# Performance work log

Measured on AMD Instinct MI355X. Metric: run time of the kernel, lower is better.

The kernel has to match this reference:

```python
import jax, jax.numpy as jnp
import numpy as np

DIM = 1024
NUM_HEADS = 16
HEAD_DIM = DIM // NUM_HEADS
SCALE = HEAD_DIM ** (-0.5)


def setup_inputs() -> dict:
    key = jax.random.key(0)
    ks = jax.random.split(key, 5)
    b, n = 4, 1370
    x = jax.random.normal(ks[0], (b, n, DIM), dtype=jnp.float32)
    # Dense kernels: Keras Dense stores kernel as [in, out]
    w_qkv = jax.random.normal(ks[1], (DIM, 3 * DIM), dtype=jnp.float32) * (DIM ** -0.5)
    b_qkv = jnp.zeros((3 * DIM,), dtype=jnp.float32)
    w_proj = jax.random.normal(ks[2], (DIM, DIM), dtype=jnp.float32) * (DIM ** -0.5)
    b_proj = jnp.zeros((DIM,), dtype=jnp.float32)
    return {"x": x, "w_qkv": w_qkv, "b_qkv": b_qkv, "w_proj": w_proj, "b_proj": b_proj}


def reference(x, w_qkv, b_qkv, w_proj, b_proj):
    b, n, _ = x.shape
    qkv = x @ w_qkv + b_qkv                       # [b, n, 3*dim]
    qkv = qkv.reshape(b, n, 3, NUM_HEADS, HEAD_DIM)
    qkv = jnp.transpose(qkv, (2, 0, 3, 1, 4))     # [3, b, h, n, d]
    q, k, v = qkv[0], qkv[1], qkv[2]
    q = q * jnp.asarray(SCALE, dtype=q.dtype)
    attn = jnp.einsum("bhqd,bhkd->bhqk", q, k)    # [b, h, n, n]
    attn = jax.nn.softmax(attn, axis=-1)
    out = jnp.einsum("bhqk,bhkd->bhqd", attn, v)  # [b, h, n, d]
    out = jnp.transpose(out, (0, 2, 1, 3)).reshape(b, n, DIM)
    return out @ w_proj + b_proj
```

## Files before the change

kernel.cpp:

```cpp
#include <hip/hip_runtime.h>
#include <stdint.h>
#include <math.h>

typedef __attribute__((ext_vector_type(8))) __bf16 bf16x8;
typedef __attribute__((ext_vector_type(4))) __bf16 bf16x4;
typedef __attribute__((ext_vector_type(4))) float f32x4;
typedef __attribute__((ext_vector_type(8))) short short8;

#define MFMA(a, b, c) __builtin_amdgcn_mfma_f32_16x16x32_bf16((a), (b), (c), 0, 0, 0)

constexpr int DIMC  = 1024;
constexpr int HEADS = 16;
constexpr int HD    = 64;
constexpr int BATCH = 4;
constexpr int SEQ   = 1370;
constexpr int MROWS = BATCH * SEQ;
constexpr int NPAD  = 1408;
constexpr float QK_SCALE = 0.125f * 1.44269504088896341f;

__device__ __forceinline__ unsigned short f2bf(float f) {
    union { float f; unsigned int u; } v; v.f = f;
    unsigned int r = (v.u + 0x7FFFu + ((v.u >> 16) & 1u)) >> 16;
    return (unsigned short)r;
}

__device__ __forceinline__ void gl2lds16(const unsigned short* g, unsigned short* l) {
    __builtin_amdgcn_global_load_lds(
        (const __attribute__((address_space(1))) unsigned int*)g,
        (__attribute__((address_space(3))) unsigned int*)l,
        16, 0, 0);
}

__global__ void cast_x_kernel(const float* __restrict__ x, unsigned short* __restrict__ xb, int nvec) {
    int i = blockIdx.x * blockDim.x + threadIdx.x;
    if (i >= nvec) return;
    f32x4 a = reinterpret_cast<const f32x4*>(x)[2 * i];
    f32x4 b = reinterpret_cast<const f32x4*>(x)[2 * i + 1];
    short8 o;
    o[0] = (short)f2bf(a[0]); o[1] = (short)f2bf(a[1]);
    o[2] = (short)f2bf(a[2]); o[3] = (short)f2bf(a[3]);
    o[4] = (short)f2bf(b[0]); o[5] = (short)f2bf(b[1]);
    o[6] = (short)f2bf(b[2]); o[7] = (short)f2bf(b[3]);
    reinterpret_cast<short8*>(xb)[i] = o;
}

__global__ __launch_bounds__(256) void transpose_cast_kernel(const float* __restrict__ in,
                                                             unsigned short* __restrict__ out,
                                                             int R, int C) {
    __shared__ float tile[32][33];
    int tx = threadIdx.x & 31, ty = threadIdx.x >> 5;
    int cbase = blockIdx.x * 32, rbase = blockIdx.y * 32;
#pragma unroll
    for (int rr = 0; rr < 4; ++rr) {
        int r = ty + rr * 8;
        tile[r][tx] = in[(size_t)(rbase + r) * C + cbase + tx];
    }
    __syncthreads();
#pragma unroll
    for (int rr = 0; rr < 4; ++rr) {
        int cr = ty + rr * 8;
        out[(size_t)(cbase + cr) * R + rbase + tx] = f2bf(tile[tx][cr]);
    }
}

__global__ void zero_vpad_kernel(unsigned short* __restrict__ vTg) {
    int idx = blockIdx.x * blockDim.x + threadIdx.x;
    const int padw = NPAD - SEQ;
    const int total = 64 * 64 * padw;
    if (idx >= total) return;
    int col = SEQ + idx % padw;
    int rowflat = idx / padw;
    vTg[(size_t)rowflat * NPAD + col] = 0;
}

template <int EPI>
__global__ __launch_bounds__(256) void gemm_bt_kernel(const unsigned short* __restrict__ A,
                                                      const unsigned short* __restrict__ Bt,
                                                      int M, int N, int K,
                                                      const float* __restrict__ bias,
                                                      unsigned short* __restrict__ qg,
                                                      unsigned short* __restrict__ kg,
                                                      unsigned short* __restrict__ vTg,
                                                      float* __restrict__ outf) {
    __shared__ unsigned short As[128 * 32];
    __shared__ unsigned short Bs[128 * 32];
    const int tid = threadIdx.x;
    const int l = tid & 63, w = tid >> 6;
    const int wr = w >> 1, wc = w & 1;
    const int lm = l & 15, lk = l >> 4;
    const int brow = blockIdx.y * 128, bcol = blockIdx.x * 128;

    f32x4 acc[4][4];
#pragma unroll
    for (int i = 0; i < 4; ++i)
#pragma unroll
        for (int j = 0; j < 4; ++j) acc[i][j] = f32x4{0.f, 0.f, 0.f, 0.f};

    const int nkt = K >> 5;
    for (int kt = 0; kt < nkt; ++kt) {
#pragma unroll
        for (int rr = 0; rr < 2; ++rr) {
            int flat = rr * 256 + tid;
            int row = flat >> 2;
            int c8 = (flat & 3) << 3;
            int ga = min(brow + row, M - 1);
            gl2lds16(&A[(size_t)ga * K + kt * 32 + c8], &As[flat * 8]);
            int gb = bcol + row;
            gl2lds16(&Bt[(size_t)gb * K + kt * 32 + c8], &Bs[flat * 8]);
        }
        __syncthreads();
        bf16x8 af[4], bfr[4];
#pragma unroll
        for (int i = 0; i < 4; ++i)
            af[i] = *reinterpret_cast<const bf16x8*>(&As[(wr * 64 + i * 16 + lm) * 32 + lk * 8]);
#pragma unroll
        for (int j = 0; j < 4; ++j)
            bfr[j] = *reinterpret_cast<const bf16x8*>(&Bs[(wc * 64 + j * 16 + lm) * 32 + lk * 8]);
#pragma unroll
        for (int i = 0; i < 4; ++i)
#pragma unroll
            for (int j = 0; j < 4; ++j)
                acc[i][j] = MFMA(af[i], bfr[j], acc[i][j]);
        __syncthreads();
    }

#pragma unroll
    for (int i = 0; i < 4; ++i) {
        int mbase = brow + wr * 64 + i * 16 + lk * 4;
#pragma unroll
        for (int j = 0; j < 4; ++j) {
            int col = bcol + wc * 64 + j * 16 + lm;
            float bv = bias[col];
#pragma unroll
            for (int r = 0; r < 4; ++r) {
                int m = mbase + r;
                if (m >= M) continue;
                float val = acc[i][j][r] + bv;
                if constexpr (EPI == 0) {
                    int which = col >> 10;
                    int head = (col >> 6) & 15;
                    int d = col & 63;
                    int b = m / SEQ;
                    int nseq = m - b * SEQ;
                    int bh = b * HEADS + head;
                    if (which == 0) {
                        qg[((size_t)bh * SEQ + nseq) * HD + d] = f2bf(val * QK_SCALE);
                    } else if (which == 1) {
                        kg[((size_t)bh * SEQ + nseq) * HD + d] = f2bf(val);
                    } else {
                        vTg[((size_t)bh * HD + d) * NPAD + nseq] = f2bf(val);
                    }
                } else {
                    outf[(size_t)m * DIMC + col] = val;
                }
            }
        }
    }
}

__global__ __launch_bounds__(256) void attn_kernel(const unsigned short* __restrict__ qg,
                                                   const unsigned short* __restrict__ kg,
                                                   const unsigned short* __restrict__ vTg,
                                                   unsigned short* __restrict__ ao) {
    __shared__ unsigned short Ks[64 * 72];
    __shared__ unsigned short Vs[64 * 72];
    __shared__ unsigned short Pw[4][16 * 72];

    const int tid = threadIdx.x;
    const int l = tid & 63, w = tid >> 6;
    const int lm = l & 15, lk = l >> 4;

    int wg = (blockIdx.x & 7) * 176 + (blockIdx.x >> 3);
    const int bh = wg / 22;
    const int qbase = (wg - bh * 22) * 64;

    int qr = min(qbase + w * 16 + lm, SEQ - 1);
    const unsigned short* qp = &qg[((size_t)bh * SEQ + qr) * HD + lk * 8];
    bf16x8 qf0 = *reinterpret_cast<const bf16x8*>(qp);
    bf16x8 qf1 = *reinterpret_cast<const bf16x8*>(qp + 32);

    f32x4 o[4];
#pragma unroll
    for (int jd = 0; jd < 4; ++jd) o[jd] = f32x4{0.f, 0.f, 0.f, 0.f};
    float mrun = -INFINITY, lrun = 0.f;

    const int r0 = tid >> 3;
    const int c8b = (tid & 7) << 3;
    const unsigned short* kbase = &kg[(size_t)bh * SEQ * HD];
    const unsigned short* vbase = &vTg[(size_t)bh * HD * NPAD];

    auto load_tile = [&](int t, short8* kr, short8* vr) {
#pragma unroll
        for (int rr = 0; rr < 2; ++rr) {
            int row = rr * 32 + r0;
            int kvg = min(t * 64 + row, SEQ - 1);
            kr[rr] = *reinterpret_cast<const short8*>(&kbase[(size_t)kvg * HD + c8b]);
            vr[rr] = *reinterpret_cast<const short8*>(&vbase[(size_t)row * NPAD + t * 64 + c8b]);
        }
    };
    auto write_tile = [&](const short8* kr, const short8* vr) {
#pragma unroll
        for (int rr = 0; rr < 2; ++rr) {
            int row = rr * 32 + r0;
            *reinterpret_cast<short8*>(&Ks[row * 72 + c8b]) = kr[rr];
            *reinterpret_cast<short8*>(&Vs[row * 72 + c8b]) = vr[rr];
        }
    };

    const int NT = (SEQ + 63) >> 6;

    auto compute_tile = [&](int t) {
        f32x4 s[4];
        __builtin_amdgcn_s_setprio(1);
#pragma unroll
        for (int j = 0; j < 4; ++j) {
            f32x4 z = {0.f, 0.f, 0.f, 0.f};
            bf16x8 k0 = *reinterpret_cast<const bf16x8*>(&Ks[(j * 16 + lm) * 72 + lk * 8]);
            bf16x8 k1 = *reinterpret_cast<const bf16x8*>(&Ks[(j * 16 + lm) * 72 + 32 + lk * 8]);
            z = MFMA(k0, qf0, z);
            z = MFMA(k1, qf1, z);
            s[j] = z;
        }
        __builtin_amdgcn_s_setprio(0);

        if (t == NT - 1) {
#pragma unroll
            for (int j = 0; j < 4; ++j)
#pragma unroll
                for (int r = 0; r < 4; ++r) {
                    int kvg = t * 64 + j * 16 + lk * 4 + r;
                    if (kvg >= SEQ) s[j][r] = -INFINITY;
                }
        }

        float tmax = s[0][0];
#pragma unroll
        for (int j = 0; j < 4; ++j)
#pragma unroll
            for (int r = 0; r < 4; ++r) tmax = fmaxf(tmax, s[j][r]);
        tmax = fmaxf(tmax, __shfl_xor(tmax, 16));
        tmax = fmaxf(tmax, __shfl_xor(tmax, 32));

        if (!__all(tmax - mrun <= 8.0f)) {
            float mnew = fmaxf(mrun, tmax);
            float scale = exp2f(mrun - mnew);
            mrun = mnew;
            lrun *= scale;
            float sc[4];
#pragma unroll
            for (int r = 0; r < 4; ++r) sc[r] = __shfl(scale, lk * 4 + r);
#pragma unroll
            for (int jd = 0; jd < 4; ++jd) {
                o[jd][0] *= sc[0]; o[jd][1] *= sc[1];
                o[jd][2] *= sc[2]; o[jd][3] *= sc[3];
            }
        }

        float p[4][4];
        float psum = 0.f;
#pragma unroll
        for (int j = 0; j < 4; ++j)
#pragma unroll
            for (int r = 0; r < 4; ++r) {
                float pv = exp2f(s[j][r] - mrun);
                p[j][r] = pv;
                psum += pv;
            }
        psum += __shfl_xor(psum, 16);
        psum += __shfl_xor(psum, 32);
        lrun += psum;

#pragma unroll
        for (int j = 0; j < 4; ++j) {
            bf16x4 pk;
            pk[0] = (__bf16)p[j][0]; pk[1] = (__bf16)p[j][1];
            pk[2] = (__bf16)p[j][2]; pk[3] = (__bf16)p[j][3];
            *reinterpret_cast<bf16x4*>(&Pw[w][lm * 72 + j * 16 + lk * 4]) = pk;
        }

        bf16x8 pa0 = *reinterpret_cast<const bf16x8*>(&Pw[w][lm * 72 + lk * 8]);
        bf16x8 pa1 = *reinterpret_cast<const bf16x8*>(&Pw[w][lm * 72 + 32 + lk * 8]);
        __builtin_amdgcn_s_setprio(1);
#pragma unroll
        for (int jd = 0; jd < 4; ++jd) {
            bf16x8 v0 = *reinterpret_cast<const bf16x8*>(&Vs[(jd * 16 + lm) * 72 + lk * 8]);
            bf16x8 v1 = *reinterpret_cast<const bf16x8*>(&Vs[(jd * 16 + lm) * 72 + 32 + lk * 8]);
            o[jd] = MFMA(pa0, v0, o[jd]);
            o[jd] = MFMA(pa1, v1, o[jd]);
        }
        __builtin_amdgcn_s_setprio(0);
    };

    short8 krA[2], vrA[2], krB[2], vrB[2];
    load_tile(0, krA, vrA);
    for (int t = 0; t < NT; t += 2) {
        write_tile(krA, vrA);
        __syncthreads();
        if (t + 1 < NT) load_tile(t + 1, krB, vrB);
        compute_tile(t);
        __syncthreads();

        write_tile(krB, vrB);
        __syncthreads();
        if (t + 2 < NT) load_tile(t + 2, krA, vrA);
        compute_tile(t + 1);
        __syncthreads();
    }

    int b = bh >> 4, h = bh & 15;
    float linv = 1.f / lrun;
#pragma unroll
    for (int r = 0; r < 4; ++r) {
        int q = qbase + w * 16 + lk * 4 + r;
        float inv = __shfl(linv, lk * 4 + r);
        if (q >= SEQ) continue;
#pragma unroll
        for (int jd = 0; jd < 4; ++jd) {
            ao[((size_t)b * SEQ + q) * DIMC + h * HD + jd * 16 + lm] = f2bf(o[jd][r] * inv);
        }
    }
}

extern "C" void kernel_launch(void* const* d_in, const int* in_sizes, int n_in,
                              void* d_out, int out_size, void* d_ws, size_t ws_size,
                              hipStream_t stream) {
    const float* x      = (const float*)d_in[0];
    const float* w_qkv  = (const float*)d_in[1];
    const float* b_qkv  = (const float*)d_in[2];
    const float* w_proj = (const float*)d_in[3];
    const float* b_proj = (const float*)d_in[4];
    float* out = (float*)d_out;

    char* ws = (char*)d_ws;
    unsigned short* xb     = (unsigned short*)ws; ws += (size_t)MROWS * DIMC * 2;
    unsigned short* wqkvT  = (unsigned short*)ws; ws += (size_t)3 * DIMC * DIMC * 2;
    unsigned short* wprojT = (unsigned short*)ws; ws += (size_t)DIMC * DIMC * 2;
    unsigned short* qg     = (unsigned short*)ws; ws += (size_t)64 * SEQ * HD * 2;
    unsigned short* kg     = (unsigned short*)ws; ws += (size_t)64 * SEQ * HD * 2;
    unsigned short* vTg    = (unsigned short*)ws; ws += (size_t)64 * HD * NPAD * 2;
    unsigned short* ao     = (unsigned short*)ws; ws += (size_t)MROWS * DIMC * 2;

    const int nvec = MROWS * DIMC / 8;
    cast_x_kernel<<<(nvec + 255) / 256, 256, 0, stream>>>(x, xb, nvec);
    transpose_cast_kernel<<<dim3(3 * DIMC / 32, DIMC / 32), 256, 0, stream>>>(w_qkv, wqkvT, DIMC, 3 * DIMC);
    transpose_cast_kernel<<<dim3(DIMC / 32, DIMC / 32), 256, 0, stream>>>(w_proj, wprojT, DIMC, DIMC);
    zero_vpad_kernel<<<(64 * 64 * (NPAD - SEQ) + 255) / 256, 256, 0, stream>>>(vTg);

    gemm_bt_kernel<0><<<dim3(3 * DIMC / 128, (MROWS + 127) / 128), 256, 0, stream>>>(
        xb, wqkvT, MROWS, 3 * DIMC, DIMC, b_qkv, qg, kg, vTg, nullptr);

    attn_kernel<<<dim3(22 * 64), 256, 0, stream>>>(qg, kg, vTg, ao);

    gemm_bt_kernel<1><<<dim3(DIMC / 128, (MROWS + 127) / 128), 256, 0, stream>>>(
        ao, wprojT, MROWS, DIMC, DIMC, b_proj, nullptr, nullptr, nullptr, out);
}
```

Measured before the change: 209.9 us.

## Double-buffer GEMM LDS tiles and load attention K/V directly from global

The GEMM kernel now uses two LDS buffers, prefetching the next K-slice while computing the current one, which removes one barrier per iteration. The attention kernel drops its shared-memory K/V staging and the barriers around it. Each wave instead reads its K and V fragments straight from global memory (relying on cache) and sets launch bounds for higher occupancy. The tradeoff is redundant global/L2 traffic, since all four waves now read the same K/V tiles, and no software prefetch in attention.

```diff
diff --git a/kernel.cpp b/kernel.cpp
--- a/kernel.cpp
+++ b/kernel.cpp
@@ -82,8 +82,8 @@
                                                       unsigned short* __restrict__ kg,
                                                       unsigned short* __restrict__ vTg,
                                                       float* __restrict__ outf) {
-    __shared__ unsigned short As[128 * 32];
-    __shared__ unsigned short Bs[128 * 32];
+    __shared__ unsigned short As[2][128 * 32];
+    __shared__ unsigned short Bs[2][128 * 32];
     const int tid = threadIdx.x;
     const int l = tid & 63, w = tid >> 6;
     const int wr = w >> 1, wc = w & 1;
@@ -96,32 +96,39 @@
 #pragma unroll
         for (int j = 0; j < 4; ++j) acc[i][j] = f32x4{0.f, 0.f, 0.f, 0.f};
 
-    const int nkt = K >> 5;
-    for (int kt = 0; kt < nkt; ++kt) {
+    auto stage = [&](int kt, int buf) {
 #pragma unroll
         for (int rr = 0; rr < 2; ++rr) {
             int flat = rr * 256 + tid;
             int row = flat >> 2;
             int c8 = (flat & 3) << 3;
             int ga = min(brow + row, M - 1);
-            gl2lds16(&A[(size_t)ga * K + kt * 32 + c8], &As[flat * 8]);
+            gl2lds16(&A[(size_t)ga * K + kt * 32 + c8], &As[buf][flat * 8]);
             int gb = bcol + row;
-            gl2lds16(&Bt[(size_t)gb * K + kt * 32 + c8], &Bs[flat * 8]);
-        }
-        __syncthreads();
+            gl2lds16(&Bt[(size_t)gb * K + kt * 32 + c8], &Bs[buf][flat * 8]);
+        }
+    };
+
+    const int nkt = K >> 5;
+    stage(0, 0);
+    __syncthreads();
+    int cur = 0;
+    for (int kt = 0; kt < nkt; ++kt) {
+        if (kt + 1 < nkt) stage(kt + 1, cur ^ 1);
         bf16x8 af[4], bfr[4];
 #pragma unroll
         for (int i = 0; i < 4; ++i)
-            af[i] = *reinterpret_cast<const bf16x8*>(&As[(wr * 64 + i * 16 + lm) * 32 + lk * 8]);
+            af[i] = *reinterpret_cast<const bf16x8*>(&As[cur][(wr * 64 + i * 16 + lm) * 32 + lk * 8]);
 #pragma unroll
         for (int j = 0; j < 4; ++j)
-            bfr[j] = *reinterpret_cast<const bf16x8*>(&Bs[(wc * 64 + j * 16 + lm) * 32 + lk * 8]);
+            bfr[j] = *reinterpret_cast<const bf16x8*>(&Bs[cur][(wc * 64 + j * 16 + lm) * 32 + lk * 8]);
 #pragma unroll
         for (int i = 0; i < 4; ++i)
 #pragma unroll
             for (int j = 0; j < 4; ++j)
                 acc[i][j] = MFMA(af[i], bfr[j], acc[i][j]);
         __syncthreads();
+        cur ^= 1;
     }
 
 #pragma unroll
@@ -158,12 +165,10 @@
     }
 }
 
-__global__ __launch_bounds__(256) void attn_kernel(const unsigned short* __restrict__ qg,
-                                                   const unsigned short* __restrict__ kg,
-                                                   const unsigned short* __restrict__ vTg,
-                                                   unsigned short* __restrict__ ao) {
-    __shared__ unsigned short Ks[64 * 72];
-    __shared__ unsigned short Vs[64 * 72];
+__global__ __launch_bounds__(256, 4) void attn_kernel(const unsigned short* __restrict__ qg,
+                                                      const unsigned short* __restrict__ kg,
+                                                      const unsigned short* __restrict__ vTg,
+                                                      unsigned short* __restrict__ ao) {
     __shared__ unsigned short Pw[4][16 * 72];
 
     const int tid = threadIdx.x;
@@ -184,44 +189,33 @@
     for (int jd = 0; jd < 4; ++jd) o[jd] = f32x4{0.f, 0.f, 0.f, 0.f};
     float mrun = -INFINITY, lrun = 0.f;
 
-    const int r0 = tid >> 3;
-    const int c8b = (tid & 7) << 3;
     const unsigned short* kbase = &kg[(size_t)bh * SEQ * HD];
     const unsigned short* vbase = &vTg[(size_t)bh * HD * NPAD];
 
-    auto load_tile = [&](int t, short8* kr, short8* vr) {
-#pragma unroll
-        for (int rr = 0; rr < 2; ++rr) {
-            int row = rr * 32 + r0;
-            int kvg = min(t * 64 + row, SEQ - 1);
-            kr[rr] = *reinterpret_cast<const short8*>(&kbase[(size_t)kvg * HD + c8b]);
-            vr[rr] = *reinterpret_cast<const short8*>(&vbase[(size_t)row * NPAD + t * 64 + c8b]);
-        }
-    };
-    auto write_tile = [&](const short8* kr, const short8* vr) {
-#pragma unroll
-        for (int rr = 0; rr < 2; ++rr) {
-            int row = rr * 32 + r0;
-            *reinterpret_cast<short8*>(&Ks[row * 72 + c8b]) = kr[rr];
-            *reinterpret_cast<short8*>(&Vs[row * 72 + c8b]) = vr[rr];
-        }
-    };
-
     const int NT = (SEQ + 63) >> 6;
-
-    auto compute_tile = [&](int t) {
+    for (int t = 0; t < NT; ++t) {
         f32x4 s[4];
         __builtin_amdgcn_s_setprio(1);
 #pragma unroll
         for (int j = 0; j < 4; ++j) {
+            int row = min(t * 64 + j * 16 + lm, SEQ - 1);
+            const unsigned short* kp = kbase + (size_t)row * HD + lk * 8;
+            bf16x8 k0 = *reinterpret_cast<const bf16x8*>(kp);
+            bf16x8 k1 = *reinterpret_cast<const bf16x8*>(kp + 32);
             f32x4 z = {0.f, 0.f, 0.f, 0.f};
-            bf16x8 k0 = *reinterpret_cast<const bf16x8*>(&Ks[(j * 16 + lm) * 72 + lk * 8]);
-            bf16x8 k1 = *reinterpret_cast<const bf16x8*>(&Ks[(j * 16 + lm) * 72 + 32 + lk * 8]);
             z = MFMA(k0, qf0, z);
             z = MFMA(k1, qf1, z);
             s[j] = z;
         }
         __builtin_amdgcn_s_setprio(0);
+
+        bf16x8 vfr[8];
+        const unsigned short* vp = vbase + t * 64 + lk * 8;
+#pragma unroll
+        for (int jd = 0; jd < 4; ++jd) {
+            vfr[2 * jd]     = *reinterpret_cast<const bf16x8*>(vp + (size_t)(jd * 16 + lm) * NPAD);
+            vfr[2 * jd + 1] = *reinterpret_cast<const bf16x8*>(vp + (size_t)(jd * 16 + lm) * NPAD + 32);
+        }
 
         if (t == NT - 1) {
 #pragma unroll
@@ -283,28 +277,10 @@
         __builtin_amdgcn_s_setprio(1);
 #pragma unroll
         for (int jd = 0; jd < 4; ++jd) {
-            bf16x8 v0 = *reinterpret_cast<const bf16x8*>(&Vs[(jd * 16 + lm) * 72 + lk * 8]);
-            bf16x8 v1 = *reinterpret_cast<const bf16x8*>(&Vs[(jd * 16 + lm) * 72 + 32 + lk * 8]);
-            o[jd] = MFMA(pa0, v0, o[jd]);
-            o[jd] = MFMA(pa1, v1, o[jd]);
+            o[jd] = MFMA(pa0, vfr[2 * jd], o[jd]);
+            o[jd] = MFMA(pa1, vfr[2 * jd + 1], o[jd]);
         }
         __builtin_amdgcn_s_setprio(0);
-    };
-
-    short8 krA[2], vrA[2], krB[2], vrB[2];
-    load_tile(0, krA, vrA);
-    for (int t = 0; t < NT; t += 2) {
-        write_tile(krA, vrA);
-        __syncthreads();
-        if (t + 1 < NT) load_tile(t + 1, krB, vrB);
-        compute_tile(t);
-        __syncthreads();
-
-        write_tile(krB, vrB);
-        __syncthreads();
-        if (t + 2 < NT) load_tile(t + 2, krA, vrA);
-        compute_tile(t + 1);
-        __syncthreads();
     }
 
     int b = bh >> 4, h = bh & 15;
```

Measured after the change: 354.7 us. 69.0% more time.
